# Kernel tuning notes

Hardware: AMD Instinct MI355X
Metric: run time of the kernel (lower is better)

Reference implementation:

```python
import jax, jax.numpy as jnp
import numpy as np

INPUT_DIMS = 512
OUTPUT_DIMS = 512
DEGREE = 7
ALPHA = 1.0


def setup_inputs() -> dict:
    key = jax.random.key(0)
    k1, k2 = jax.random.split(key)
    x = jax.random.normal(k1, (16384, INPUT_DIMS), dtype=jnp.float32)
    std = 1.0 / (INPUT_DIMS * (DEGREE + 1))
    coeffs = jax.random.normal(k2, (INPUT_DIMS, OUTPUT_DIMS, DEGREE + 1), dtype=jnp.float32) * std
    return {"x": x, "gegenbauer_coeffs": coeffs}


def reference(x, gegenbauer_coeffs):
    # x: (B, I) -> tanh squashed into (-1, 1) domain of Gegenbauer polys
    x = jnp.tanh(x.reshape(-1, INPUT_DIMS))
    a = ALPHA
    polys = [jnp.ones_like(x)]
    if DEGREE > 0:
        polys.append(2.0 * a * x)
    # recurrence: C_{n+1} = (2(n+a) x C_n - (n+2a-1) C_{n-1}) / (n+1)
    for n in range(1, DEGREE):
        polys.append((2.0 * (n + a) * x * polys[n] - (n + 2.0 * a - 1.0) * polys[n - 1]) / (n + 1.0))
    g = jnp.stack(polys, axis=-1)  # (B, I, D+1)
    y = jnp.einsum('bid,iod->bo', g, gegenbauer_coeffs)
    return y.reshape(-1, OUTPUT_DIMS)
```

## Files before the change

### kernel.cpp

```cpp
#include <hip/hip_runtime.h>
#include <hip/hip_bf16.h>


#define I_DIM 512
#define O_DIM 512
#define NDEG 8
#define BM 64
#define BN 256
#define IPB 8
#define LSTR 72
#define KITERS (I_DIM / IPB)
#define NTHREADS 256
#define W_ELEMS (I_DIM * O_DIM * NDEG)

typedef __attribute__((ext_vector_type(8))) short s8v;
typedef __attribute__((ext_vector_type(4))) float f32x4;
typedef unsigned short u16;

__device__ __forceinline__ unsigned cvt_pk_bf16(float lo, float hi) {
    unsigned r;
    asm("v_cvt_pk_bf16_f32 %0, %1, %2" : "=v"(r) : "v"(lo), "v"(hi));
    return r;
}

__device__ __forceinline__ float fast_tanh(float v) {
    float e = __expf(v + v);
    float r = __builtin_amdgcn_rcpf(e + 1.0f);
    return 1.0f - (r + r);
}

extern "C" __global__ __launch_bounds__(256)
void cvt_w(const float* __restrict__ cf, u16* __restrict__ wbf) {
    const size_t idx = ((size_t)blockIdx.x * 256 + threadIdx.x) * 4;
    const float4 v = *reinterpret_cast<const float4*>(cf + idx);
    unsigned* dst = reinterpret_cast<unsigned*>(wbf + idx);
    dst[0] = cvt_pk_bf16(v.x, v.y);
    dst[1] = cvt_pk_bf16(v.z, v.w);
}

template <bool PRECONV>
__global__ __launch_bounds__(NTHREADS, 3)
void gegen_gemm(const float* __restrict__ x,
                const float* __restrict__ cf,
                const u16* __restrict__ wbf,
                float* __restrict__ out)
{
    __shared__ u16 As[BM * LSTR];
    __shared__ u16 Ws[IPB * BN * NDEG];

    const int tid  = threadIdx.x;
    const int lane = tid & 63;
    const int wave = tid >> 6;
    const int fm   = lane & 15;
    const int fq   = lane >> 4;
    const int wr   = ((wave >> 1) & 1) << 5;
    const int wc   = (wave & 1) << 7;

    const int bm0 = blockIdx.y * BM;
    const int bn0 = blockIdx.x * BN;

    const int ar = tid >> 2;
    const int ai = (tid & 3) << 1;
    const float* xp = x + (size_t)(bm0 + ar) * I_DIM + ai;

    f32x4 acc[2][8];
#pragma unroll
    for (int a = 0; a < 2; ++a)
#pragma unroll
        for (int b = 0; b < 8; ++b)
            acc[a][b] = (f32x4){0.0f, 0.0f, 0.0f, 0.0f};

    for (int it = 0; it < KITERS; ++it) {
        if (PRECONV) {
            const u16* wsrc = wbf + ((size_t)(it * IPB) * O_DIM + bn0) * NDEG;
#pragma unroll
            for (int q = 0; q < 8; ++q) {
                const int c    = wave * 8 + q;
                const int il   = c >> 2;
                const int qt   = c & 3;
                const u16* src = wsrc + ((size_t)il * O_DIM + qt * 64 + lane) * NDEG;
                u16* dst = &Ws[(il * BN + qt * 64) * NDEG];
                __builtin_amdgcn_global_load_lds(
                    (const __attribute__((address_space(1))) void*)src,
                    (__attribute__((address_space(3))) void*)dst, 16, 0, 0);
            }
        } else {
#pragma unroll
            for (int jj = 0; jj < 8; ++jj) {
                const int p  = jj * NTHREADS + tid;
                const int il = p >> 8;
                const int o  = p & 255;
                const float* src = cf + ((size_t)(it * IPB + il) * O_DIM + bn0 + o) * NDEG;
                const float4 w0 = reinterpret_cast<const float4*>(src)[0];
                const float4 w1 = reinterpret_cast<const float4*>(src)[1];
                union { s8v s; unsigned u[4]; } pk;
                pk.u[0] = cvt_pk_bf16(w0.x, w0.y);
                pk.u[1] = cvt_pk_bf16(w0.z, w0.w);
                pk.u[2] = cvt_pk_bf16(w1.x, w1.y);
                pk.u[3] = cvt_pk_bf16(w1.z, w1.w);
                *reinterpret_cast<s8v*>(&Ws[(il * BN + o) * NDEG]) = pk.s;
            }
        }

        {
            const float2 xv = *reinterpret_cast<const float2*>(xp + it * IPB);
            const float vv[2] = {xv.x, xv.y};
#pragma unroll
            for (int j = 0; j < 2; ++j) {
                const float t  = fast_tanh(vv[j]);
                const float t2 = t + t;
                const float c1 = t2;
                const float c2 = t2 * c1 - 1.0f;
                const float c3 = t2 * c2 - c1;
                const float c4 = t2 * c3 - c2;
                const float c5 = t2 * c4 - c3;
                const float c6 = t2 * c5 - c4;
                const float c7 = t2 * c6 - c5;
                union { s8v s; unsigned u[4]; } pk;
                pk.u[0] = cvt_pk_bf16(1.0f, c1);
                pk.u[1] = cvt_pk_bf16(c2, c3);
                pk.u[2] = cvt_pk_bf16(c4, c5);
                pk.u[3] = cvt_pk_bf16(c6, c7);
                *reinterpret_cast<s8v*>(&As[ar * LSTR + (ai + j) * NDEG]) = pk.s;
            }
        }
        __syncthreads();

#pragma unroll
        for (int kc = 0; kc < 2; ++kc) {
            s8v afr[2], bfr[8];
#pragma unroll
            for (int tm = 0; tm < 2; ++tm)
                afr[tm] = *reinterpret_cast<const s8v*>(
                    &As[(wr + tm * 16 + fm) * LSTR + kc * 32 + fq * 8]);
#pragma unroll
            for (int tn = 0; tn < 8; ++tn)
                bfr[tn] = *reinterpret_cast<const s8v*>(
                    &Ws[((kc * 4 + fq) * BN + wc + tn * 16 + fm) * NDEG]);
#pragma unroll
            for (int tm = 0; tm < 2; ++tm)
#pragma unroll
                for (int tn = 0; tn < 8; ++tn)
                    acc[tm][tn] = __builtin_amdgcn_mfma_f32_16x16x32_bf16(
                        afr[tm], bfr[tn], acc[tm][tn], 0, 0, 0);
        }
        __syncthreads();
    }

#pragma unroll
    for (int tm = 0; tm < 2; ++tm) {
#pragma unroll
        for (int tn = 0; tn < 8; ++tn) {
            const int row = bm0 + wr + tm * 16 + fq * 4;
            const int col = bn0 + wc + tn * 16 + fm;
#pragma unroll
            for (int r = 0; r < 4; ++r)
                out[(size_t)(row + r) * O_DIM + col] = acc[tm][tn][r];
        }
    }
}

extern "C" void kernel_launch(void* const* d_in, const int* in_sizes, int n_in,
                              void* d_out, int out_size, void* d_ws, size_t ws_size,
                              hipStream_t stream) {
    const float* x  = (const float*)d_in[0];
    const float* cf = (const float*)d_in[1];
    float* out = (float*)d_out;
    const int M = in_sizes[0] / I_DIM;
    dim3 grid(O_DIM / BN, M / BM);
    dim3 block(NTHREADS, 1, 1);

    if (ws_size >= (size_t)W_ELEMS * sizeof(u16)) {
        u16* wbf = (u16*)d_ws;
        cvt_w<<<W_ELEMS / 1024, 256, 0, stream>>>(cf, wbf);
        gegen_gemm<true><<<grid, block, 0, stream>>>(x, cf, wbf, out);
    } else {
        gegen_gemm<false><<<grid, block, 0, stream>>>(x, cf, nullptr, out);
    }
}
```

Baseline: 159.9 us.

## Drop LDS staging; load fragments directly from global per wave

Removes shared-memory staging and both block barriers. Each wave now owns a 64x128 output tile and loads its weight fragments straight from global memory into registers, computing the polynomial features in registers. The grid is remapped to 64x4 blocks of 256 threads, with a larger accumulator (4x8 MFMA tiles) per wave. Sharing across the waves in a block is lost, so global and L2 traffic for weights rises, the x loads are uncoalesced scalar loads, and the larger accumulator raises register pressure.

Result: slower. 211.9 us (+32.5%).

```diff
diff --git a/kernel.cpp b/kernel.cpp
--- a/kernel.cpp
+++ b/kernel.cpp
@@ -5,12 +5,7 @@
 #define I_DIM 512
 #define O_DIM 512
 #define NDEG 8
-#define BM 64
-#define BN 256
-#define IPB 8
-#define LSTR 72
-#define KITERS (I_DIM / IPB)
-#define NTHREADS 256
+#define KITERS 64
 #define W_ELEMS (I_DIM * O_DIM * NDEG)
 
 typedef __attribute__((ext_vector_type(8))) short s8v;
@@ -29,6 +24,24 @@
     return 1.0f - (r + r);
 }
 
+__device__ __forceinline__ s8v feat_frag(float xv) {
+    const float t  = fast_tanh(xv);
+    const float t2 = t + t;
+    const float c1 = t2;
+    const float c2 = t2 * c1 - 1.0f;
+    const float c3 = t2 * c2 - c1;
+    const float c4 = t2 * c3 - c2;
+    const float c5 = t2 * c4 - c3;
+    const float c6 = t2 * c5 - c4;
+    const float c7 = t2 * c6 - c5;
+    union { s8v s; unsigned u[4]; } pk;
+    pk.u[0] = cvt_pk_bf16(1.0f, c1);
+    pk.u[1] = cvt_pk_bf16(c2, c3);
+    pk.u[2] = cvt_pk_bf16(c4, c5);
+    pk.u[3] = cvt_pk_bf16(c6, c7);
+    return pk.s;
+}
+
 extern "C" __global__ __launch_bounds__(256)
 void cvt_w(const float* __restrict__ cf, u16* __restrict__ wbf) {
     const size_t idx = ((size_t)blockIdx.x * 256 + threadIdx.x) * 4;
@@ -39,120 +52,84 @@
 }
 
 template <bool PRECONV>
-__global__ __launch_bounds__(NTHREADS, 3)
+__global__ __launch_bounds__(256, 2)
 void gegen_gemm(const float* __restrict__ x,
                 const float* __restrict__ cf,
                 const u16* __restrict__ wbf,
                 float* __restrict__ out)
 {
-    __shared__ u16 As[BM * LSTR];
-    __shared__ u16 Ws[IPB * BN * NDEG];
-
     const int tid  = threadIdx.x;
     const int lane = tid & 63;
     const int wave = tid >> 6;
     const int fm   = lane & 15;
     const int fq   = lane >> 4;
-    const int wr   = ((wave >> 1) & 1) << 5;
-    const int wc   = (wave & 1) << 7;
 
-    const int bm0 = blockIdx.y * BM;
-    const int bn0 = blockIdx.x * BN;
+    const int bm0 = blockIdx.x * 256 + wave * 64;
+    const int bn0 = blockIdx.y * 128;
 
-    const int ar = tid >> 2;
-    const int ai = (tid & 3) << 1;
-    const float* xp = x + (size_t)(bm0 + ar) * I_DIM + ai;
+    const float* xr0 = x + (size_t)(bm0 +  0 + fm) * I_DIM;
+    const float* xr1 = x + (size_t)(bm0 + 16 + fm) * I_DIM;
+    const float* xr2 = x + (size_t)(bm0 + 32 + fm) * I_DIM;
+    const float* xr3 = x + (size_t)(bm0 + 48 + fm) * I_DIM;
 
-    f32x4 acc[2][8];
+    f32x4 acc[4][8];
 #pragma unroll
-    for (int a = 0; a < 2; ++a)
+    for (int a = 0; a < 4; ++a)
 #pragma unroll
         for (int b = 0; b < 8; ++b)
             acc[a][b] = (f32x4){0.0f, 0.0f, 0.0f, 0.0f};
 
     for (int it = 0; it < KITERS; ++it) {
-        if (PRECONV) {
-            const u16* wsrc = wbf + ((size_t)(it * IPB) * O_DIM + bn0) * NDEG;
 #pragma unroll
-            for (int q = 0; q < 8; ++q) {
-                const int c    = wave * 8 + q;
-                const int il   = c >> 2;
-                const int qt   = c & 3;
-                const u16* src = wsrc + ((size_t)il * O_DIM + qt * 64 + lane) * NDEG;
-                u16* dst = &Ws[(il * BN + qt * 64) * NDEG];
-                __builtin_amdgcn_global_load_lds(
-                    (const __attribute__((address_space(1))) void*)src,
-                    (__attribute__((address_space(3))) void*)dst, 16, 0, 0);
+        for (int kc = 0; kc < 2; ++kc) {
+            const int i0 = it * 8 + kc * 4 + fq;
+
+            s8v bfr[8];
+            if (PRECONV) {
+                const u16* wb = wbf + ((size_t)i0 * O_DIM + bn0 + fm) * NDEG;
+#pragma unroll
+                for (int tn = 0; tn < 8; ++tn)
+                    bfr[tn] = *reinterpret_cast<const s8v*>(wb + (size_t)tn * 16 * NDEG);
+            } else {
+                const float* wb = cf + ((size_t)i0 * O_DIM + bn0 + fm) * NDEG;
+#pragma unroll
+                for (int tn = 0; tn < 8; ++tn) {
+                    const float4 w0 = reinterpret_cast<const float4*>(wb + (size_t)tn * 16 * NDEG)[0];
+                    const float4 w1 = reinterpret_cast<const float4*>(wb + (size_t)tn * 16 * NDEG)[1];
+                    union { s8v s; unsigned u[4]; } pk;
+                    pk.u[0] = cvt_pk_bf16(w0.x, w0.y);
+                    pk.u[1] = cvt_pk_bf16(w0.z, w0.w);
+                    pk.u[2] = cvt_pk_bf16(w1.x, w1.y);
+                    pk.u[3] = cvt_pk_bf16(w1.z, w1.w);
+                    bfr[tn] = pk.s;
+                }
             }
-        } else {
-#pragma unroll
-            for (int jj = 0; jj < 8; ++jj) {
-                const int p  = jj * NTHREADS + tid;
-                const int il = p >> 8;
-                const int o  = p & 255;
-                const float* src = cf + ((size_t)(it * IPB + il) * O_DIM + bn0 + o) * NDEG;
-                const float4 w0 = reinterpret_cast<const float4*>(src)[0];
-                const float4 w1 = reinterpret_cast<const float4*>(src)[1];
-                union { s8v s; unsigned u[4]; } pk;
-                pk.u[0] = cvt_pk_bf16(w0.x, w0.y);
-                pk.u[1] = cvt_pk_bf16(w0.z, w0.w);
-                pk.u[2] = cvt_pk_bf16(w1.x, w1.y);
-                pk.u[3] = cvt_pk_bf16(w1.z, w1.w);
-                *reinterpret_cast<s8v*>(&Ws[(il * BN + o) * NDEG]) = pk.s;
-            }
-        }
 
-        {
-            const float2 xv = *reinterpret_cast<const float2*>(xp + it * IPB);
-            const float vv[2] = {xv.x, xv.y};
-#pragma unroll
-            for (int j = 0; j < 2; ++j) {
-                const float t  = fast_tanh(vv[j]);
-                const float t2 = t + t;
-                const float c1 = t2;
-                const float c2 = t2 * c1 - 1.0f;
-                const float c3 = t2 * c2 - c1;
-                const float c4 = t2 * c3 - c2;
-                const float c5 = t2 * c4 - c3;
-                const float c6 = t2 * c5 - c4;
-                const float c7 = t2 * c6 - c5;
-                union { s8v s; unsigned u[4]; } pk;
-                pk.u[0] = cvt_pk_bf16(1.0f, c1);
-                pk.u[1] = cvt_pk_bf16(c2, c3);
-                pk.u[2] = cvt_pk_bf16(c4, c5);
-                pk.u[3] = cvt_pk_bf16(c6, c7);
-                *reinterpret_cast<s8v*>(&As[ar * LSTR + (ai + j) * NDEG]) = pk.s;
-            }
-        }
-        __syncthreads();
+            const float x0 = xr0[i0];
+            const float x1 = xr1[i0];
+            const float x2 = xr2[i0];
+            const float x3 = xr3[i0];
+            s8v afr[4];
+            afr[0] = feat_frag(x0);
+            afr[1] = feat_frag(x1);
+            afr[2] = feat_frag(x2);
+            afr[3] = feat_frag(x3);
 
 #pragma unroll
-        for (int kc = 0; kc < 2; ++kc) {
-            s8v afr[2], bfr[8];
-#pragma unroll
-            for (int tm = 0; tm < 2; ++tm)
-                afr[tm] = *reinterpret_cast<const s8v*>(
-                    &As[(wr + tm * 16 + fm) * LSTR + kc * 32 + fq * 8]);
-#pragma unroll
-            for (int tn = 0; tn < 8; ++tn)
-                bfr[tn] = *reinterpret_cast<const s8v*>(
-                    &Ws[((kc * 4 + fq) * BN + wc + tn * 16 + fm) * NDEG]);
-#pragma unroll
-            for (int tm = 0; tm < 2; ++tm)
+            for (int tm = 0; tm < 4; ++tm)
 #pragma unroll
                 for (int tn = 0; tn < 8; ++tn)
                     acc[tm][tn] = __builtin_amdgcn_mfma_f32_16x16x32_bf16(
                         afr[tm], bfr[tn], acc[tm][tn], 0, 0, 0);
         }
-        __syncthreads();
     }
 
 #pragma unroll
-    for (int tm = 0; tm < 2; ++tm) {
+    for (int tm = 0; tm < 4; ++tm) {
 #pragma unroll
         for (int tn = 0; tn < 8; ++tn) {
-            const int row = bm0 + wr + tm * 16 + fq * 4;
-            const int col = bn0 + wc + tn * 16 + fm;
+            const int row = bm0 + tm * 16 + fq * 4;
+            const int col = bn0 + tn * 16 + fm;
 #pragma unroll
             for (int r = 0; r < 4; ++r)
                 out[(size_t)(row + r) * O_DIM + col] = acc[tm][tn][r];
@@ -167,8 +144,8 @@
     const float* cf = (const float*)d_in[1];
     float* out = (float*)d_out;
     const int M = in_sizes[0] / I_DIM;
-    dim3 grid(O_DIM / BN, M / BM);
-    dim3 block(NTHREADS, 1, 1);
+    dim3 grid(M / 256, O_DIM / 128);
+    dim3 block(256, 1, 1);
 
     if (ws_size >= (size_t)W_ELEMS * sizeof(u16)) {
         u16* wbf = (u16*)d_ws;
```
